# Performance work log

Measured on AMD Instinct MI355X. Metric: run time of the kernel, lower is better.

The kernel has to match this reference:

```python
import jax, jax.numpy as jnp
import numpy as np

B, N, D, H = 1, 4096, 1024, 16
E = D // H  # head_dim = 64


def setup_inputs() -> dict:
    key = jax.random.key(0)
    ks = jax.random.split(key, 5)
    s = 0.02
    return {
        "query": jax.random.normal(ks[0], (B, N, D), dtype=jnp.float32),
        "Wq": jax.random.normal(ks[1], (D, D), dtype=jnp.float32) * s,
        "Wk": jax.random.normal(ks[2], (D, D), dtype=jnp.float32) * s,
        "Wv": jax.random.normal(ks[3], (D, D), dtype=jnp.float32) * s,
        "Wo": jax.random.normal(ks[4], (D, D), dtype=jnp.float32) * s,
        "bo": jnp.zeros((D,), dtype=jnp.float32),
    }


def reference(query, Wq, Wk, Wv, Wo, bo):
    # self-attention: key = value = query
    # nn.Linear: y = x @ W.T  (weights stored as [out, in])
    q = query @ Wq.T  # [b, n, d]
    k = query @ Wk.T
    v = query @ Wv.T
    # 'b n (h e) -> b h n e'
    q = q.reshape(B, N, H, E).transpose(0, 2, 1, 3)
    k = k.reshape(B, N, H, E).transpose(0, 2, 1, 3)
    v = v.reshape(B, N, H, E).transpose(0, 2, 1, 3)
    scale = 1.0 / jnp.sqrt(jnp.asarray(E, dtype=q.dtype))
    attn = jnp.einsum('bhne,bhme->bhnm', q, k) * scale  # [b, h, n, n]
    attn = jax.nn.softmax(attn, axis=-1)
    out = jnp.einsum('bhnm,bhme->bhne', attn, v)  # [b, h, n, e]
    # 'b h n e -> b n (h e)'
    out = out.transpose(0, 2, 1, 3).reshape(B, N, D)
    out = out @ Wo.T + bo
    return out
```

## Files before the change

### kernel.cpp

```cpp
#include <hip/hip_runtime.h>


typedef __attribute__((ext_vector_type(8))) __bf16 bf16x8;
typedef __attribute__((ext_vector_type(4))) float f32x4;
typedef __attribute__((ext_vector_type(16))) float f32x16;
typedef __attribute__((ext_vector_type(4))) unsigned short us4;
typedef __attribute__((ext_vector_type(4))) unsigned int u32x4;
typedef __attribute__((ext_vector_type(2))) unsigned int u32x2;

#define DEV __device__ __forceinline__

#define QSCALE 0.1803368801111204f

DEV unsigned short f2bf(float x) {
  union { float f; unsigned u; } c; c.f = x;
  unsigned u = c.u;
  u += 0x7FFFu + ((u >> 16) & 1u);
  return (unsigned short)(u >> 16);
}

DEV float expq(float x) {
#if __has_builtin(__builtin_amdgcn_exp2f)
  return __builtin_amdgcn_exp2f(x);
#else
  float r;
  asm("v_exp_f32 %0, %1" : "=v"(r) : "v"(x));
  return r;
#endif
}

DEV unsigned cvtpk_bf16(float lo, float hi) {
  unsigned r;
  asm("v_cvt_pk_bf16_f32 %0, %1, %2" : "=v"(r) : "v"(lo), "v"(hi));
  return r;
}

DEV void plswap_u(unsigned& a, unsigned& b) {
#if __has_builtin(__builtin_amdgcn_permlane32_swap)
  u32x2 r = __builtin_amdgcn_permlane32_swap(a, b, false, false);
  a = r.x; b = r.y;
#else
  asm("v_permlane32_swap_b32 %0, %1" : "+v"(a), "+v"(b));
#endif
}

DEV void plswap_f(float& a, float& b) {
  unsigned ua = __float_as_uint(a), ub = __float_as_uint(b);
  plswap_u(ua, ub);
  a = __uint_as_float(ua); b = __uint_as_float(ub);
}

DEV void gload16(const void* g, void* lds) {
  __builtin_amdgcn_global_load_lds(
      (const __attribute__((address_space(1))) unsigned int*)g,
      (__attribute__((address_space(3))) unsigned int*)lds, 16, 0, 0);
}

__global__ void cast_all(const float* __restrict__ q,
                         const float* __restrict__ wa,
                         const float* __restrict__ wb,
                         const float* __restrict__ wc,
                         const float* __restrict__ wd,
                         unsigned short* __restrict__ qo,
                         unsigned short* __restrict__ wout) {
  const int y = blockIdx.y;
  const int i = blockIdx.x * 256 + threadIdx.x;
  const float* src;
  unsigned short* dst;
  if (y < 4) {
    src = q + (size_t)y * 1048576;
    dst = qo + (size_t)y * 1048576;
  } else {
    src = (y == 4) ? wa : (y == 5) ? wb : (y == 6) ? wc : wd;
    dst = wout + (size_t)(y - 4) * 1048576;
  }
  float4 v = reinterpret_cast<const float4*>(src)[i];
  us4 o;
  o.x = f2bf(v.x); o.y = f2bf(v.y); o.z = f2bf(v.z); o.w = f2bf(v.w);
  reinterpret_cast<us4*>(dst)[i] = o;
}

__global__ __launch_bounds__(256)
void gemm_qkv(const unsigned short* __restrict__ A,
              const unsigned short* __restrict__ B,
              unsigned short* __restrict__ Qo,
              unsigned short* __restrict__ Ko,
              unsigned short* __restrict__ Vo) {
  constexpr int K = 1024, BK = 64;
  __shared__ unsigned short As[128 * BK];
  __shared__ unsigned short Bs[128 * BK];
  const int t = threadIdx.x;
  const int w = t >> 6, l = t & 63;
  const int brow = blockIdx.x * 128;
  const int bcol = blockIdx.y * 128;
  const int wr = w >> 1, wc = w & 1;
  const int lr = l >> 3;
  const int lc = ((l & 7) ^ lr) * 8;
  const int fr = l & 15;
  const int fcb = (l >> 4) * 16;
  const int swz = (l & 7) << 4;

  f32x4 acc[4][4] = {};
  const char* Asb = (const char*)As;
  const char* Bsb = (const char*)Bs;

  for (int k0 = 0; k0 < K; k0 += BK) {
#pragma unroll
    for (int i = 0; i < 4; ++i) {
      const int r = w * 32 + i * 8;
      gload16(A + (size_t)(brow + r + lr) * K + k0 + lc, (void*)(As + r * BK));
      gload16(B + (size_t)(bcol + r + lr) * K + k0 + lc, (void*)(Bs + r * BK));
    }
    __syncthreads();
#pragma unroll
    for (int kk = 0; kk < 2; ++kk) {
      bf16x8 af[4], bfr[4];
#pragma unroll
      for (int m = 0; m < 4; ++m)
        af[m] = *(const bf16x8*)(Asb + (wr * 64 + m * 16 + fr) * 128 +
                                 ((kk * 64 + fcb) ^ swz));
#pragma unroll
      for (int n = 0; n < 4; ++n)
        bfr[n] = *(const bf16x8*)(Bsb + (wc * 64 + n * 16 + fr) * 128 +
                                  ((kk * 64 + fcb) ^ swz));
#pragma unroll
      for (int m = 0; m < 4; ++m)
#pragma unroll
        for (int n = 0; n < 4; ++n)
          acc[m][n] = __builtin_amdgcn_mfma_f32_16x16x32_bf16(
              af[m], bfr[n], acc[m][n], 0, 0, 0);
    }
    __syncthreads();
  }

  const int seg = blockIdx.y >> 3;
  const int orow = brow + wr * 64 + (l >> 4) * 4;
  const int ocol = (blockIdx.y & 7) * 128 + wc * 64 + fr;
  if (seg == 1) {
#pragma unroll
    for (int n = 0; n < 4; ++n) {
      const int C = ocol + n * 16;
      const int bn = (C >> 6) * 262144 + ((C & 63) >> 3) * 512 + (C & 7);
#pragma unroll
      for (int m = 0; m < 4; ++m)
#pragma unroll
        for (int j = 0; j < 4; ++j) {
          const int R = orow + m * 16 + j;
          Ko[bn + (R >> 6) * 4096 + (R & 63) * 8] = f2bf(acc[m][n][j]);
        }
    }
  } else if (seg == 2) {
#pragma unroll
    for (int n = 0; n < 4; ++n) {
      const int C = ocol + n * 16;
      const int bn = (C >> 6) * 262144 + (C & 63) * 8;
#pragma unroll
      for (int m = 0; m < 4; ++m) {
        const int R0 = orow + m * 16;
        us4 o4;
        o4.x = f2bf(acc[m][n][0]); o4.y = f2bf(acc[m][n][1]);
        o4.z = f2bf(acc[m][n][2]); o4.w = f2bf(acc[m][n][3]);
        *(us4*)(Vo + bn + (R0 >> 6) * 4096 + ((R0 & 63) >> 3) * 512 + (R0 & 7)) = o4;
      }
    }
  } else {
#pragma unroll
    for (int m = 0; m < 4; ++m)
#pragma unroll
      for (int n = 0; n < 4; ++n)
#pragma unroll
        for (int j = 0; j < 4; ++j)
          Qo[(size_t)(orow + m * 16 + j) * 1024 + (ocol + n * 16)] =
              f2bf(acc[m][n][j] * QSCALE);
  }
}

__global__ __launch_bounds__(256)
void gemm_out64(const unsigned short* __restrict__ A,
                const unsigned short* __restrict__ B,
                float* __restrict__ C, const float* __restrict__ bias) {
  constexpr int N = 1024, K = 1024, BK = 64;
  __shared__ unsigned short As[64 * BK];
  __shared__ unsigned short Bs[128 * BK];
  const int t = threadIdx.x;
  const int w = t >> 6, l = t & 63;
  const int brow = blockIdx.x * 64;
  const int bcol = blockIdx.y * 128;
  const int wr = w >> 1, wc = w & 1;
  const int lr = l >> 3;
  const int lc = ((l & 7) ^ lr) * 8;
  const int fr = l & 15;
  const int fcb = (l >> 4) * 16;
  const int swz = (l & 7) << 4;

  f32x4 acc[2][4] = {};
  const char* Asb = (const char*)As;
  const char* Bsb = (const char*)Bs;

  for (int k0 = 0; k0 < K; k0 += BK) {
#pragma unroll
    for (int i = 0; i < 2; ++i) {
      const int r = w * 16 + i * 8;
      gload16(A + (size_t)(brow + r + lr) * K + k0 + lc, (void*)(As + r * BK));
    }
#pragma unroll
    for (int i = 0; i < 4; ++i) {
      const int r = w * 32 + i * 8;
      gload16(B + (size_t)(bcol + r + lr) * K + k0 + lc, (void*)(Bs + r * BK));
    }
    __syncthreads();
#pragma unroll
    for (int kk = 0; kk < 2; ++kk) {
      bf16x8 af[2], bfr[4];
#pragma unroll
      for (int m = 0; m < 2; ++m)
        af[m] = *(const bf16x8*)(Asb + (wr * 32 + m * 16 + fr) * 128 +
                                 ((kk * 64 + fcb) ^ swz));
#pragma unroll
      for (int n = 0; n < 4; ++n)
        bfr[n] = *(const bf16x8*)(Bsb + (wc * 64 + n * 16 + fr) * 128 +
                                  ((kk * 64 + fcb) ^ swz));
#pragma unroll
      for (int m = 0; m < 2; ++m)
#pragma unroll
        for (int n = 0; n < 4; ++n)
          acc[m][n] = __builtin_amdgcn_mfma_f32_16x16x32_bf16(
              af[m], bfr[n], acc[m][n], 0, 0, 0);
    }
    __syncthreads();
  }

  const int orow = brow + wr * 32 + (l >> 4) * 4;
  const int ocol = bcol + wc * 64 + fr;
#pragma unroll
  for (int m = 0; m < 2; ++m)
#pragma unroll
    for (int n = 0; n < 4; ++n)
#pragma unroll
      for (int j = 0; j < 4; ++j)
        C[(size_t)(orow + m * 16 + j) * N + (ocol + n * 16)] =
            acc[m][n][j] + bias[ocol + n * 16];
}

__global__ __launch_bounds__(512, 4)
void attn_v15(const unsigned short* __restrict__ Q,
              const unsigned short* __restrict__ Kp,
              const unsigned short* __restrict__ Vp,
              unsigned short* __restrict__ AO) {
  constexpr int D = 1024, NIT = 64;
  __shared__ unsigned long long LDSA[51200 / 8];
  char* LDS = (char*)LDSA;
  const int t = threadIdx.x, w = t >> 6, l = t & 63;
  const int g = w >> 2, wg = w & 3;
  const int flat = blockIdx.x;
  const int c = flat & 7, ii = flat >> 3;
  const int h = c * 2 + (ii >> 5);
  const int qt = ii & 31;
  const int q0 = qt * 128 + wg * 32;
  const int ln = l & 31, hi = l >> 5;
  const int lr = l >> 3;

  char* kgrp = LDS + g * 12288;
  char* vgrp = LDS + 24576 + g * 12288;

  bf16x8 qf[4];
  {
    const unsigned short* qp = Q + (size_t)(q0 + ln) * D + h * 64 + hi * 8;
#pragma unroll
    for (int ks = 0; ks < 4; ++ks) qf[ks] = *(const bf16x8*)(qp + ks * 16);
  }

  f32x16 oacc0 = {}, oacc1 = {};
  float lsum = 0.f;

  const char* KgL = (const char*)Kp + (size_t)(h * 64) * 8192 + g * 512 +
                    (wg * 2 + (l >> 5)) * 1024 + (l & 31) * 16;
  const char* VgL = (const char*)Vp + (size_t)(h * 64) * 8192 + g * 4096 +
                    wg * 1024 + l * 16;
  char* kdst = kgrp + wg * 1024;
  char* vdst = vgrp + wg * 1024;

  auto stage = [&](int buf, int it) {
    const size_t o = (size_t)it * 8192;
    gload16(KgL + o, kdst + buf * 4096);
    gload16(VgL + o, vdst + buf * 4096);
  };

  stage(0, 0);
  stage(1, 1);

  for (int i = 0; i < NIT; ++i) {
    if (i < NIT - 2)
      asm volatile("s_waitcnt vmcnt(2)" ::: "memory");
    else
      asm volatile("s_waitcnt vmcnt(0)" ::: "memory");
    __builtin_amdgcn_s_barrier();
    if (i + 2 < NIT) stage((i + 2) % 3, i + 2);

    const char* ksb = kgrp + (i % 3) * 4096;
    const char* vsb = vgrp + (i % 3) * 4096;

    f32x16 sa = {};
    __builtin_amdgcn_s_setprio(1);
#pragma unroll
    for (int ks = 0; ks < 4; ++ks) {
      bf16x8 kf = *(const bf16x8*)(ksb + (2 * ks + hi) * 512 + ln * 16);
      sa = __builtin_amdgcn_mfma_f32_32x32x16_bf16(kf, qf[ks], sa, 0, 0, 0);
    }
    __builtin_amdgcn_s_setprio(0);

#pragma unroll
    for (int r = 0; r < 16; ++r) sa[r] = expq(sa[r]);
    {
      float red[8];
#pragma unroll
      for (int r = 0; r < 8; ++r) red[r] = sa[r] + sa[r + 8];
#pragma unroll
      for (int s = 4; s >= 1; s >>= 1)
#pragma unroll
        for (int r = 0; r < s; ++r) red[r] += red[r + s];
      lsum += red[0];
    }

    unsigned pw[2][4];
#pragma unroll
    for (int kvs = 0; kvs < 2; ++kvs) {
      const int rb = kvs * 8;
      unsigned A0 = cvtpk_bf16(sa[rb + 0], sa[rb + 1]);
      unsigned B0 = cvtpk_bf16(sa[rb + 4], sa[rb + 5]);
      unsigned A1 = cvtpk_bf16(sa[rb + 2], sa[rb + 3]);
      unsigned B1 = cvtpk_bf16(sa[rb + 6], sa[rb + 7]);
      plswap_u(A0, B0);
      plswap_u(A1, B1);
      pw[kvs][0] = A0; pw[kvs][1] = A1; pw[kvs][2] = B0; pw[kvs][3] = B1;
    }

    __builtin_amdgcn_s_setprio(1);
#pragma unroll
    for (int kvs = 0; kvs < 2; ++kvs) {
      u32x4 pv = {pw[kvs][0], pw[kvs][1], pw[kvs][2], pw[kvs][3]};
      bf16x8 pf = __builtin_bit_cast(bf16x8, pv);
      bf16x8 vf0 = *(const bf16x8*)(vsb + (2 * kvs + hi) * 1024 + ln * 16);
      bf16x8 vf1 = *(const bf16x8*)(vsb + (2 * kvs + hi) * 1024 + 512 + ln * 16);
      oacc0 = __builtin_amdgcn_mfma_f32_32x32x16_bf16(vf0, pf, oacc0, 0, 0, 0);
      oacc1 = __builtin_amdgcn_mfma_f32_32x32x16_bf16(vf1, pf, oacc1, 0, 0, 0);
    }
    __builtin_amdgcn_s_setprio(0);
  }

  __syncthreads();

  float* cb = (float*)LDS;
  float* cl = (float*)(LDS + 32768);
  if (g == 1) {
    float* p = cb + (wg * 64 + l) * 32;
#pragma unroll
    for (int r = 0; r < 16; ++r) { p[r] = oacc0[r]; p[16 + r] = oacc1[r]; }
    cl[wg * 64 + l] = lsum;
  }
  __syncthreads();
  if (g == 0) {
    float* p = cb + (wg * 64 + l) * 32;
#pragma unroll
    for (int r = 0; r < 16; ++r) { oacc0[r] += p[r]; oacc1[r] += p[16 + r]; }
    lsum += cl[wg * 64 + l];
    float sa2 = lsum, sb2 = lsum;
    plswap_f(sa2, sb2);
    const float inv = 1.0f / (sa2 + sb2);

    char* Osc = LDS + 34816 + wg * 4096;
#pragma unroll
    for (int es = 0; es < 2; ++es)
#pragma unroll
      for (int gg = 0; gg < 4; ++gg)
#pragma unroll
        for (int c2 = 0; c2 < 2; ++c2) {
          const f32x16& oa = es == 0 ? oacc0 : oacc1;
          unsigned pk = cvtpk_bf16(oa[gg * 4 + c2 * 2] * inv,
                                   oa[gg * 4 + c2 * 2 + 1] * inv);
          const int col = es * 64 + gg * 16 + hi * 8 + c2 * 4;
          *(unsigned*)(Osc + ln * 128 + (col ^ ((ln & 7) << 4))) = pk;
        }
#pragma unroll
    for (int p2 = 0; p2 < 4; ++p2) {
      const int q = p2 * 8 + lr;
      bf16x8 ov = *(const bf16x8*)(Osc + q * 128 + (((l & 7) ^ lr) << 4));
      *(bf16x8*)(AO + (size_t)(q0 + q) * D + h * 64 + (l & 7) * 8) = ov;
    }
  }
}

extern "C" void kernel_launch(void* const* d_in, const int* in_sizes, int n_in,
                              void* d_out, int out_size, void* d_ws, size_t ws_size,
                              hipStream_t stream) {
  const float* query = (const float*)d_in[0];
  const float* Wq    = (const float*)d_in[1];
  const float* Wk    = (const float*)d_in[2];
  const float* Wv    = (const float*)d_in[3];
  const float* Wo    = (const float*)d_in[4];
  const float* bo    = (const float*)d_in[5];
  float* out = (float*)d_out;

  char* ws = (char*)d_ws;
  const size_t MB = 1024 * 1024;
  unsigned short* Wqkv_b = (unsigned short*)(ws + 0 * MB);
  unsigned short* Wo_b   = (unsigned short*)(ws + 6 * MB);
  unsigned short* Xb     = (unsigned short*)(ws + 8 * MB);
  unsigned short* Qb     = (unsigned short*)(ws + 16 * MB);
  unsigned short* Kb     = (unsigned short*)(ws + 24 * MB);
  unsigned short* Vtb    = (unsigned short*)(ws + 40 * MB);
  unsigned short* AOb    = (unsigned short*)(ws + 32 * MB);

  cast_all<<<dim3(1024, 8), dim3(256), 0, stream>>>(query, Wq, Wk, Wv, Wo,
                                                    Xb, Wqkv_b);

  gemm_qkv<<<dim3(32, 24), dim3(256), 0, stream>>>(Xb, Wqkv_b, Qb, Kb, Vtb);

  attn_v15<<<dim3(512), dim3(512), 0, stream>>>(Qb, Kb, Vtb, AOb);

  gemm_out64<<<dim3(64, 8), dim3(256), 0, stream>>>(AOb, Wo_b, out, bo);
}
```

Baseline: 145.7 us.

## Software-pipeline QK^T of next KV tile with softmax and PV of current

Restructures the attention inner loop so the QK^T MFMAs for tile i+1 are issued alongside the exp, bf16 packing and PV MFMAs for tile i. Two score accumulators alternate across a loop unrolled by two, and a prologue computes the first tile's scores. The vmcnt waits are relaxed so each iteration waits for the next K tile and the current V tile instead of whole stages. This aims to hide the dependency stall between score MFMAs and the exp/convert work, at the cost of an extra 16-register accumulator that may raise register pressure at 512 threads.

```diff
diff --git a/kernel.cpp b/kernel.cpp
--- a/kernel.cpp
+++ b/kernel.cpp
@@ -242,8 +242,59 @@
             acc[m][n][j] + bias[ocol + n * 16];
 }
 
+
+#define AITER(I, SCUR, SNXT) do { \
+    if ((I) < NIT - 2) asm volatile("s_waitcnt vmcnt(1)" ::: "memory"); \
+    else               asm volatile("s_waitcnt vmcnt(0)" ::: "memory"); \
+    __builtin_amdgcn_s_barrier(); \
+    if ((I) + 2 < NIT) stage(((I) + 2) % 3, (I) + 2); \
+     \
+    _Pragma("unroll") for (int r = 0; r < 16; ++r) (SCUR)[r] = expq((SCUR)[r]); \
+    { \
+      float red[8]; \
+      _Pragma("unroll") for (int r = 0; r < 8; ++r) red[r] = (SCUR)[r] + (SCUR)[r + 8]; \
+      _Pragma("unroll") for (int s = 4; s >= 1; s >>= 1) \
+        _Pragma("unroll") for (int r = 0; r < s; ++r) red[r] += red[r + s]; \
+      lsum += red[0]; \
+    } \
+    unsigned pw[2][4]; \
+    _Pragma("unroll") for (int kvs = 0; kvs < 2; ++kvs) { \
+      const int rb = kvs * 8; \
+      unsigned A0 = cvtpk_bf16((SCUR)[rb + 0], (SCUR)[rb + 1]); \
+      unsigned B0 = cvtpk_bf16((SCUR)[rb + 4], (SCUR)[rb + 5]); \
+      unsigned A1 = cvtpk_bf16((SCUR)[rb + 2], (SCUR)[rb + 3]); \
+      unsigned B1 = cvtpk_bf16((SCUR)[rb + 6], (SCUR)[rb + 7]); \
+      plswap_u(A0, B0); \
+      plswap_u(A1, B1); \
+      pw[kvs][0] = A0; pw[kvs][1] = A1; pw[kvs][2] = B0; pw[kvs][3] = B1; \
+    } \
+     \
+    __builtin_amdgcn_s_setprio(1); \
+    if ((I) + 1 < NIT) { \
+      const char* kn_ = kgrp + (((I) + 1) % 3) * 4096; \
+      f32x16 z_ = {}; \
+      (SNXT) = z_; \
+      _Pragma("unroll") for (int ks = 0; ks < 4; ++ks) { \
+        bf16x8 kf = *(const bf16x8*)(kn_ + (2 * ks + hi) * 512 + ln * 16); \
+        (SNXT) = __builtin_amdgcn_mfma_f32_32x32x16_bf16(kf, qf[ks], (SNXT), 0, 0, 0); \
+      } \
+    } \
+    { \
+      const char* vsb_ = vgrp + ((I) % 3) * 4096; \
+      _Pragma("unroll") for (int kvs = 0; kvs < 2; ++kvs) { \
+        u32x4 pv = {pw[kvs][0], pw[kvs][1], pw[kvs][2], pw[kvs][3]}; \
+        bf16x8 pf = __builtin_bit_cast(bf16x8, pv); \
+        bf16x8 vf0 = *(const bf16x8*)(vsb_ + (2 * kvs + hi) * 1024 + ln * 16); \
+        bf16x8 vf1 = *(const bf16x8*)(vsb_ + (2 * kvs + hi) * 1024 + 512 + ln * 16); \
+        oacc0 = __builtin_amdgcn_mfma_f32_32x32x16_bf16(vf0, pf, oacc0, 0, 0, 0); \
+        oacc1 = __builtin_amdgcn_mfma_f32_32x32x16_bf16(vf1, pf, oacc1, 0, 0, 0); \
+      } \
+    } \
+    __builtin_amdgcn_s_setprio(0); \
+  } while (0)
+
 __global__ __launch_bounds__(512, 4)
-void attn_v15(const unsigned short* __restrict__ Q,
+void attn_v16(const unsigned short* __restrict__ Q,
               const unsigned short* __restrict__ Kp,
               const unsigned short* __restrict__ Vp,
               unsigned short* __restrict__ AO) {
@@ -289,63 +340,18 @@
   stage(0, 0);
   stage(1, 1);
 
-  for (int i = 0; i < NIT; ++i) {
-    if (i < NIT - 2)
-      asm volatile("s_waitcnt vmcnt(2)" ::: "memory");
-    else
-      asm volatile("s_waitcnt vmcnt(0)" ::: "memory");
-    __builtin_amdgcn_s_barrier();
-    if (i + 2 < NIT) stage((i + 2) % 3, i + 2);
-
-    const char* ksb = kgrp + (i % 3) * 4096;
-    const char* vsb = vgrp + (i % 3) * 4096;
-
-    f32x16 sa = {};
-    __builtin_amdgcn_s_setprio(1);
-#pragma unroll
-    for (int ks = 0; ks < 4; ++ks) {
-      bf16x8 kf = *(const bf16x8*)(ksb + (2 * ks + hi) * 512 + ln * 16);
-      sa = __builtin_amdgcn_mfma_f32_32x32x16_bf16(kf, qf[ks], sa, 0, 0, 0);
-    }
-    __builtin_amdgcn_s_setprio(0);
-
-#pragma unroll
-    for (int r = 0; r < 16; ++r) sa[r] = expq(sa[r]);
-    {
-      float red[8];
-#pragma unroll
-      for (int r = 0; r < 8; ++r) red[r] = sa[r] + sa[r + 8];
-#pragma unroll
-      for (int s = 4; s >= 1; s >>= 1)
-#pragma unroll
-        for (int r = 0; r < s; ++r) red[r] += red[r + s];
-      lsum += red[0];
-    }
-
-    unsigned pw[2][4];
-#pragma unroll
-    for (int kvs = 0; kvs < 2; ++kvs) {
-      const int rb = kvs * 8;
-      unsigned A0 = cvtpk_bf16(sa[rb + 0], sa[rb + 1]);
-      unsigned B0 = cvtpk_bf16(sa[rb + 4], sa[rb + 5]);
-      unsigned A1 = cvtpk_bf16(sa[rb + 2], sa[rb + 3]);
-      unsigned B1 = cvtpk_bf16(sa[rb + 6], sa[rb + 7]);
-      plswap_u(A0, B0);
-      plswap_u(A1, B1);
-      pw[kvs][0] = A0; pw[kvs][1] = A1; pw[kvs][2] = B0; pw[kvs][3] = B1;
-    }
-
-    __builtin_amdgcn_s_setprio(1);
-#pragma unroll
-    for (int kvs = 0; kvs < 2; ++kvs) {
-      u32x4 pv = {pw[kvs][0], pw[kvs][1], pw[kvs][2], pw[kvs][3]};
-      bf16x8 pf = __builtin_bit_cast(bf16x8, pv);
-      bf16x8 vf0 = *(const bf16x8*)(vsb + (2 * kvs + hi) * 1024 + ln * 16);
-      bf16x8 vf1 = *(const bf16x8*)(vsb + (2 * kvs + hi) * 1024 + 512 + ln * 16);
-      oacc0 = __builtin_amdgcn_mfma_f32_32x32x16_bf16(vf0, pf, oacc0, 0, 0, 0);
-      oacc1 = __builtin_amdgcn_mfma_f32_32x32x16_bf16(vf1, pf, oacc1, 0, 0, 0);
-    }
-    __builtin_amdgcn_s_setprio(0);
+  asm volatile("s_waitcnt vmcnt(3)" ::: "memory");
+  __builtin_amdgcn_s_barrier();
+  f32x16 saA = {}, saB = {};
+#pragma unroll
+  for (int ks = 0; ks < 4; ++ks) {
+    bf16x8 kf = *(const bf16x8*)(kgrp + (2 * ks + hi) * 512 + ln * 16);
+    saA = __builtin_amdgcn_mfma_f32_32x32x16_bf16(kf, qf[ks], saA, 0, 0, 0);
+  }
+
+  for (int i = 0; i < NIT; i += 2) {
+    AITER(i, saA, saB);
+    AITER(i + 1, saB, saA);
   }
 
   __syncthreads();
@@ -416,7 +422,7 @@
 
   gemm_qkv<<<dim3(32, 24), dim3(256), 0, stream>>>(Xb, Wqkv_b, Qb, Kb, Vtb);
 
-  attn_v15<<<dim3(512), dim3(512), 0, stream>>>(Qb, Kb, Vtb, AOb);
+  attn_v16<<<dim3(512), dim3(512), 0, stream>>>(Qb, Kb, Vtb, AOb);
 
   gemm_out64<<<dim3(64, 8), dim3(256), 0, stream>>>(AOb, Wo_b, out, bo);
 }
```

After: 147.9 us. No clear change (+1.5%).
